# Kernel tuning notes

Hardware: AMD Instinct MI355X
Metric: run time of the kernel (lower is better)

## Reference

```python
import jax, jax.numpy as jnp
import numpy as np


def setup_inputs() -> dict:
    key = jax.random.key(0)
    k1, k2, k3 = jax.random.split(key, 3)
    B, T, F, U = 32, 4096, 512, 512
    x = jax.random.normal(k1, (B, T, F), dtype=jnp.float32)
    W = jax.random.normal(k2, (F, U), dtype=jnp.float32)
    b = jnp.zeros((U,), dtype=jnp.float32)
    V = jax.random.uniform(k3, (U, 1), dtype=jnp.float32)
    return {"x": x, "W": W, "b": b, "V": V}


def reference(x, W, b, V):
    # u = tanh(x @ W + b): [B, T, U]
    u = jnp.tanh(jnp.einsum('btf,fu->btu', x, W) + b)
    # scores = u @ V: [B, T, 1]; softmax over time (dim=1)
    a = jax.nn.softmax(jnp.einsum('btu,uo->bto', u, V), axis=1)
    # weighted sum pooling over time -> [B, F]
    return jnp.sum(x * a, axis=1)
```

## Files before the change

kernel.cpp:

```cpp
#include <hip/hip_runtime.h>


#define XT 4096
#define XF 512
#define XU 512
#define ROWS (32 * 4096)

typedef __attribute__((ext_vector_type(8))) short short8;
typedef __attribute__((ext_vector_type(16))) float f32x16;

__device__ inline void cvt_hilo(float x, unsigned short &h, unsigned short &l) {
  unsigned u = __builtin_bit_cast(unsigned, x);
  h = (unsigned short)(u >> 16);
  float hf = __builtin_bit_cast(float, u & 0xFFFF0000u);
  float lo = x - hf;
  l = (unsigned short)(__builtin_bit_cast(unsigned, lo) >> 16);
}

__device__ inline float tanh_fast(float z) {
  float e = __expf(2.0f * z);
  return 1.0f - 2.0f * __builtin_amdgcn_rcpf(e + 1.0f);
}

__global__ void wconv_kernel(const float *__restrict__ W,
                             unsigned short *__restrict__ whi,
                             unsigned short *__restrict__ wlo) {
  int t2 = blockIdx.x * 256 + threadIdx.x;
  int l = t2 & 31;
  int g = (t2 >> 5) & 1;
  int t = (t2 >> 6) & 15;
  int s = t2 >> 10;
  short8 hv, lv;
#pragma unroll
  for (int j = 0; j < 8; ++j) {
    unsigned short h, lo;
    cvt_hilo(W[(size_t)(s * 16 + g * 8 + j) * XU + t * 32 + l], h, lo);
    hv[j] = (short)h;
    lv[j] = (short)lo;
  }
  size_t off = (size_t)s * 8192 + t * 512 + g * 256 + l * 8;
  *(short8 *)(whi + off) = hv;
  *(short8 *)(wlo + off) = lv;
}

__global__ __launch_bounds__(512, 2)
void gemm_scores_kernel(const float *__restrict__ x,
                        const unsigned short *__restrict__ whi,
                        const unsigned short *__restrict__ wlo,
                        const float *__restrict__ bias,
                        const float *__restrict__ V,
                        float *__restrict__ scores) {
  __shared__ float scb[512];

  const int tid = threadIdx.x;
  const int lane = tid & 63;
  const int wave = tid >> 6;
  const int wr = wave >> 2;
  const int wc = wave & 3;
  const int l31 = lane & 31;
  const int half = lane >> 5;
  const size_t rowbase = (size_t)blockIdx.x * 128;

  f32x16 acc[2][4];
#pragma unroll
  for (int a = 0; a < 2; ++a)
#pragma unroll
    for (int c = 0; c < 4; ++c)
#pragma unroll
      for (int r = 0; r < 16; ++r) acc[a][c][r] = 0.f;

  const float *xr0 = x + (rowbase + wr * 64 + l31) * XF + half * 8;
  const float *xr1 = xr0 + 32 * XF;
  const unsigned short *whp = whi + (size_t)(wc * 4) * 512 + lane * 8;
  const unsigned short *wlp = wlo + (size_t)(wc * 4) * 512 + lane * 8;

#pragma unroll 1
  for (int s = 0; s < 32; ++s) {
    short8 bh[4], bl[4];
    const unsigned short *p = whp + (size_t)s * 8192;
    const unsigned short *q = wlp + (size_t)s * 8192;
#pragma unroll
    for (int cf = 0; cf < 4; ++cf) {
      bh[cf] = *(const short8 *)(p + cf * 512);
      bl[cf] = *(const short8 *)(q + cf * 512);
    }
    float4 a00 = *(const float4 *)(xr0 + s * 16);
    float4 a01 = *(const float4 *)(xr0 + s * 16 + 4);
    float4 a10 = *(const float4 *)(xr1 + s * 16);
    float4 a11 = *(const float4 *)(xr1 + s * 16 + 4);

    short8 ah0, al0, ah1, al1;
    {
      float v0[8] = {a00.x, a00.y, a00.z, a00.w, a01.x, a01.y, a01.z, a01.w};
      float v1[8] = {a10.x, a10.y, a10.z, a10.w, a11.x, a11.y, a11.z, a11.w};
#pragma unroll
      for (int j = 0; j < 8; ++j) {
        unsigned short h, lo;
        cvt_hilo(v0[j], h, lo);
        ah0[j] = (short)h; al0[j] = (short)lo;
        cvt_hilo(v1[j], h, lo);
        ah1[j] = (short)h; al1[j] = (short)lo;
      }
    }

#pragma unroll
    for (int cf = 0; cf < 4; ++cf) {
      acc[0][cf] = __builtin_amdgcn_mfma_f32_32x32x16_bf16(ah0, bh[cf], acc[0][cf], 0, 0, 0);
      acc[1][cf] = __builtin_amdgcn_mfma_f32_32x32x16_bf16(ah1, bh[cf], acc[1][cf], 0, 0, 0);
      acc[0][cf] = __builtin_amdgcn_mfma_f32_32x32x16_bf16(al0, bh[cf], acc[0][cf], 0, 0, 0);
      acc[1][cf] = __builtin_amdgcn_mfma_f32_32x32x16_bf16(al1, bh[cf], acc[1][cf], 0, 0, 0);
      acc[0][cf] = __builtin_amdgcn_mfma_f32_32x32x16_bf16(ah0, bl[cf], acc[0][cf], 0, 0, 0);
      acc[1][cf] = __builtin_amdgcn_mfma_f32_32x32x16_bf16(ah1, bl[cf], acc[1][cf], 0, 0, 0);
    }
  }

  float sc[2][16];
#pragma unroll
  for (int rf = 0; rf < 2; ++rf)
#pragma unroll
    for (int r = 0; r < 16; ++r) sc[rf][r] = 0.f;

#pragma unroll
  for (int cf = 0; cf < 4; ++cf) {
    int n = wc * 128 + cf * 32 + l31;
    float vv = V[n];
    float bb = bias[n];
#pragma unroll
    for (int rf = 0; rf < 2; ++rf)
#pragma unroll
      for (int r = 0; r < 16; ++r)
        sc[rf][r] += tanh_fast(acc[rf][cf][r] + bb) * vv;
  }
#pragma unroll
  for (int m = 1; m <= 16; m <<= 1) {
#pragma unroll
    for (int rf = 0; rf < 2; ++rf)
#pragma unroll
      for (int r = 0; r < 16; ++r)
        sc[rf][r] += __shfl_xor(sc[rf][r], m, 64);
  }
  if (l31 == 0) {
#pragma unroll
    for (int rf = 0; rf < 2; ++rf)
#pragma unroll
      for (int r = 0; r < 16; ++r) {
        int row = wr * 64 + rf * 32 + (r & 3) + 8 * (r >> 2) + 4 * half;
        scb[wc * 128 + row] = sc[rf][r];
      }
  }
  __syncthreads();
  if (tid < 128)
    scores[rowbase + tid] =
        scb[tid] + scb[128 + tid] + scb[256 + tid] + scb[384 + tid];
}

__global__ void stats_kernel(const float *__restrict__ scores,
                             float *__restrict__ stats) {
  int b = blockIdx.x, tid = threadIdx.x;
  const float *s = scores + (size_t)b * XT;
  float v[16];
#pragma unroll
  for (int i = 0; i < 16; ++i) v[i] = s[tid + i * 256];
  float mx = v[0];
#pragma unroll
  for (int i = 1; i < 16; ++i) mx = fmaxf(mx, v[i]);
  for (int m = 1; m < 64; m <<= 1) mx = fmaxf(mx, __shfl_xor(mx, m, 64));
  __shared__ float redm[4], reds[4];
  if ((tid & 63) == 0) redm[tid >> 6] = mx;
  __syncthreads();
  mx = fmaxf(fmaxf(redm[0], redm[1]), fmaxf(redm[2], redm[3]));
  float sum = 0.f;
#pragma unroll
  for (int i = 0; i < 16; ++i) sum += __expf(v[i] - mx);
  for (int m = 1; m < 64; m <<= 1) sum += __shfl_xor(sum, m, 64);
  if ((tid & 63) == 0) reds[tid >> 6] = sum;
  __syncthreads();
  if (tid == 0) {
    stats[b * 2] = mx;
    stats[b * 2 + 1] = reds[0] + reds[1] + reds[2] + reds[3];
  }
}

__global__ __launch_bounds__(256)
void pool_kernel(const float *__restrict__ x, const float *__restrict__ scores,
                 const float *__restrict__ stats, float *__restrict__ out) {
  int b = blockIdx.x >> 5;
  int ch = blockIdx.x & 31;
  int tid = threadIdx.x;
  __shared__ float w[128];
  __shared__ float red[512];
  float mx = stats[b * 2];
  float inv = 1.0f / stats[b * 2 + 1];
  if (tid < 128)
    w[tid] = __expf(scores[(size_t)b * XT + ch * 128 + tid] - mx) * inv;
  __syncthreads();
  int c = tid & 127;
  int ro = tid >> 7;
  const float *xp = x + ((size_t)b * XT + ch * 128) * XF;
  float4 a = {0.f, 0.f, 0.f, 0.f};
#pragma unroll 4
  for (int i = 0; i < 64; ++i) {
    int r = i * 2 + ro;
    float4 v = *(const float4 *)(xp + (size_t)r * XF + c * 4);
    float wv = w[r];
    a.x += wv * v.x;
    a.y += wv * v.y;
    a.z += wv * v.z;
    a.w += wv * v.w;
  }
  if (ro == 1) {
    red[c * 4 + 0] = a.x;
    red[c * 4 + 1] = a.y;
    red[c * 4 + 2] = a.z;
    red[c * 4 + 3] = a.w;
  }
  __syncthreads();
  if (ro == 0) {
    atomicAdd(&out[b * XF + c * 4 + 0], a.x + red[c * 4 + 0]);
    atomicAdd(&out[b * XF + c * 4 + 1], a.y + red[c * 4 + 1]);
    atomicAdd(&out[b * XF + c * 4 + 2], a.z + red[c * 4 + 2]);
    atomicAdd(&out[b * XF + c * 4 + 3], a.w + red[c * 4 + 3]);
  }
}

extern "C" void kernel_launch(void *const *d_in, const int *in_sizes, int n_in,
                              void *d_out, int out_size, void *d_ws,
                              size_t ws_size, hipStream_t stream) {
  const float *x = (const float *)d_in[0];
  const float *W = (const float *)d_in[1];
  const float *bias = (const float *)d_in[2];
  const float *V = (const float *)d_in[3];
  float *out = (float *)d_out;

  unsigned short *whi = (unsigned short *)d_ws;
  unsigned short *wlo = whi + 262144;
  float *scores = (float *)((char *)d_ws + 1048576);
  float *stats = (float *)((char *)d_ws + 1572864);

  hipMemsetAsync(d_out, 0, (size_t)out_size * sizeof(float), stream);
  wconv_kernel<<<128, 256, 0, stream>>>(W, whi, wlo);
  gemm_scores_kernel<<<1024, 512, 0, stream>>>(x, whi, wlo, bias, V, scores);
  stats_kernel<<<32, 256, 0, stream>>>(scores, stats);
  pool_kernel<<<1024, 256, 0, stream>>>(x, scores, stats, out);
}
```

Baseline: 572.9 us.

## Software-pipeline GEMM loads and conversion; halve pool chunk size

The GEMM main loop now double-buffers the W-hi fragments and raw x rows, prefetching step s+1 while issuing MFMAs for step s, and converts x for the next step after the MFMAs. A perm-based cvt_row packs the bf16 hi/lo halves two at a time, and the MFMAs are regrouped by operand. The pool kernel uses 64-row chunks over 2048 blocks for more parallelism, at the cost of twice as many atomics. The extra buffers raise register pressure under the 2-blocks-per-CU launch bound.

```diff
diff --git a/kernel.cpp b/kernel.cpp
--- a/kernel.cpp
+++ b/kernel.cpp
@@ -4,17 +4,40 @@
 #define XT 4096
 #define XF 512
 #define XU 512
-#define ROWS (32 * 4096)
 
 typedef __attribute__((ext_vector_type(8))) short short8;
 typedef __attribute__((ext_vector_type(16))) float f32x16;
+typedef __attribute__((ext_vector_type(4))) unsigned int u32x4;
+
+__device__ inline unsigned fbits(float x) { return __builtin_bit_cast(unsigned, x); }
+__device__ inline float bitsf(unsigned u) { return __builtin_bit_cast(float, u); }
 
 __device__ inline void cvt_hilo(float x, unsigned short &h, unsigned short &l) {
-  unsigned u = __builtin_bit_cast(unsigned, x);
+  unsigned u = fbits(x);
   h = (unsigned short)(u >> 16);
-  float hf = __builtin_bit_cast(float, u & 0xFFFF0000u);
-  float lo = x - hf;
-  l = (unsigned short)(__builtin_bit_cast(unsigned, lo) >> 16);
+  float lo = x - bitsf(u & 0xFFFF0000u);
+  l = (unsigned short)(fbits(lo) >> 16);
+}
+
+__device__ inline unsigned hipack(unsigned a, unsigned b) {
+  return __builtin_amdgcn_perm(b, a, 0x07060302u);
+}
+
+__device__ inline void cvt_row(float4 c0, float4 c1, short8 &h8, short8 &l8) {
+  float f[8] = {c0.x, c0.y, c0.z, c0.w, c1.x, c1.y, c1.z, c1.w};
+  unsigned hp[4], lp[4];
+#pragma unroll
+  for (int p = 0; p < 4; ++p) {
+    unsigned u0 = fbits(f[2 * p]), u1 = fbits(f[2 * p + 1]);
+    hp[p] = hipack(u0, u1);
+    float l0 = f[2 * p] - bitsf(u0 & 0xFFFF0000u);
+    float l1 = f[2 * p + 1] - bitsf(u1 & 0xFFFF0000u);
+    lp[p] = hipack(fbits(l0), fbits(l1));
+  }
+  u32x4 hv = {hp[0], hp[1], hp[2], hp[3]};
+  u32x4 lv = {lp[0], lp[1], lp[2], lp[3]};
+  h8 = __builtin_bit_cast(short8, hv);
+  l8 = __builtin_bit_cast(short8, lv);
 }
 
 __device__ inline float tanh_fast(float z) {
@@ -43,6 +66,8 @@
   *(short8 *)(wlo + off) = lv;
 }
 
+#define MFMA(a, b, c) __builtin_amdgcn_mfma_f32_32x32x16_bf16(a, b, c, 0, 0, 0)
+
 __global__ __launch_bounds__(512, 2)
 void gemm_scores_kernel(const float *__restrict__ x,
                         const unsigned short *__restrict__ whi,
@@ -74,44 +99,51 @@
   const unsigned short *whp = whi + (size_t)(wc * 4) * 512 + lane * 8;
   const unsigned short *wlp = wlo + (size_t)(wc * 4) * 512 + lane * 8;
 
-#pragma unroll 1
+  short8 bh[2][4], bl[4];
+  float4 raw[2][4];
+  short8 ah0, al0, ah1, al1;
+
+#pragma unroll
+  for (int cf = 0; cf < 4; ++cf) bh[0][cf] = *(const short8 *)(whp + cf * 512);
+  raw[0][0] = *(const float4 *)(xr0);
+  raw[0][1] = *(const float4 *)(xr0 + 4);
+  raw[0][2] = *(const float4 *)(xr1);
+  raw[0][3] = *(const float4 *)(xr1 + 4);
+  cvt_row(raw[0][0], raw[0][1], ah0, al0);
+  cvt_row(raw[0][2], raw[0][3], ah1, al1);
+
+#pragma unroll 2
   for (int s = 0; s < 32; ++s) {
-    short8 bh[4], bl[4];
-    const unsigned short *p = whp + (size_t)s * 8192;
-    const unsigned short *q = wlp + (size_t)s * 8192;
+    const int cur = s & 1, nxt = cur ^ 1;
+    const int sn = (s + 1) & 31;
+#pragma unroll
+    for (int cf = 0; cf < 4; ++cf)
+      bl[cf] = *(const short8 *)(wlp + (size_t)s * 8192 + cf * 512);
+#pragma unroll
+    for (int cf = 0; cf < 4; ++cf)
+      bh[nxt][cf] = *(const short8 *)(whp + (size_t)sn * 8192 + cf * 512);
+    raw[nxt][0] = *(const float4 *)(xr0 + sn * 16);
+    raw[nxt][1] = *(const float4 *)(xr0 + sn * 16 + 4);
+    raw[nxt][2] = *(const float4 *)(xr1 + sn * 16);
+    raw[nxt][3] = *(const float4 *)(xr1 + sn * 16 + 4);
+
 #pragma unroll
     for (int cf = 0; cf < 4; ++cf) {
-      bh[cf] = *(const short8 *)(p + cf * 512);
-      bl[cf] = *(const short8 *)(q + cf * 512);
+      acc[0][cf] = MFMA(ah0, bh[cur][cf], acc[0][cf]);
+      acc[1][cf] = MFMA(ah1, bh[cur][cf], acc[1][cf]);
     }
-    float4 a00 = *(const float4 *)(xr0 + s * 16);
-    float4 a01 = *(const float4 *)(xr0 + s * 16 + 4);
-    float4 a10 = *(const float4 *)(xr1 + s * 16);
-    float4 a11 = *(const float4 *)(xr1 + s * 16 + 4);
-
-    short8 ah0, al0, ah1, al1;
-    {
-      float v0[8] = {a00.x, a00.y, a00.z, a00.w, a01.x, a01.y, a01.z, a01.w};
-      float v1[8] = {a10.x, a10.y, a10.z, a10.w, a11.x, a11.y, a11.z, a11.w};
-#pragma unroll
-      for (int j = 0; j < 8; ++j) {
-        unsigned short h, lo;
-        cvt_hilo(v0[j], h, lo);
-        ah0[j] = (short)h; al0[j] = (short)lo;
-        cvt_hilo(v1[j], h, lo);
-        ah1[j] = (short)h; al1[j] = (short)lo;
-      }
+#pragma unroll
+    for (int cf = 0; cf < 4; ++cf) {
+      acc[0][cf] = MFMA(al0, bh[cur][cf], acc[0][cf]);
+      acc[1][cf] = MFMA(al1, bh[cur][cf], acc[1][cf]);
     }
-
 #pragma unroll
     for (int cf = 0; cf < 4; ++cf) {
-      acc[0][cf] = __builtin_amdgcn_mfma_f32_32x32x16_bf16(ah0, bh[cf], acc[0][cf], 0, 0, 0);
-      acc[1][cf] = __builtin_amdgcn_mfma_f32_32x32x16_bf16(ah1, bh[cf], acc[1][cf], 0, 0, 0);
-      acc[0][cf] = __builtin_amdgcn_mfma_f32_32x32x16_bf16(al0, bh[cf], acc[0][cf], 0, 0, 0);
-      acc[1][cf] = __builtin_amdgcn_mfma_f32_32x32x16_bf16(al1, bh[cf], acc[1][cf], 0, 0, 0);
-      acc[0][cf] = __builtin_amdgcn_mfma_f32_32x32x16_bf16(ah0, bl[cf], acc[0][cf], 0, 0, 0);
-      acc[1][cf] = __builtin_amdgcn_mfma_f32_32x32x16_bf16(ah1, bl[cf], acc[1][cf], 0, 0, 0);
+      acc[0][cf] = MFMA(ah0, bl[cf], acc[0][cf]);
+      acc[1][cf] = MFMA(ah1, bl[cf], acc[1][cf]);
     }
+    cvt_row(raw[nxt][0], raw[nxt][1], ah0, al0);
+    cvt_row(raw[nxt][2], raw[nxt][3], ah1, al1);
   }
 
   float sc[2][16];
@@ -184,22 +216,22 @@
 __global__ __launch_bounds__(256)
 void pool_kernel(const float *__restrict__ x, const float *__restrict__ scores,
                  const float *__restrict__ stats, float *__restrict__ out) {
-  int b = blockIdx.x >> 5;
-  int ch = blockIdx.x & 31;
+  int b = blockIdx.x >> 6;
+  int ch = blockIdx.x & 63;
   int tid = threadIdx.x;
-  __shared__ float w[128];
+  __shared__ float w[64];
   __shared__ float red[512];
   float mx = stats[b * 2];
   float inv = 1.0f / stats[b * 2 + 1];
-  if (tid < 128)
-    w[tid] = __expf(scores[(size_t)b * XT + ch * 128 + tid] - mx) * inv;
+  if (tid < 64)
+    w[tid] = __expf(scores[(size_t)b * XT + ch * 64 + tid] - mx) * inv;
   __syncthreads();
   int c = tid & 127;
   int ro = tid >> 7;
-  const float *xp = x + ((size_t)b * XT + ch * 128) * XF;
+  const float *xp = x + ((size_t)b * XT + ch * 64) * XF;
   float4 a = {0.f, 0.f, 0.f, 0.f};
-#pragma unroll 4
-  for (int i = 0; i < 64; ++i) {
+#pragma unroll 8
+  for (int i = 0; i < 32; ++i) {
     int r = i * 2 + ro;
     float4 v = *(const float4 *)(xp + (size_t)r * XF + c * 4);
     float wv = w[r];
@@ -241,5 +273,5 @@
   wconv_kernel<<<128, 256, 0, stream>>>(W, whi, wlo);
   gemm_scores_kernel<<<1024, 512, 0, stream>>>(x, whi, wlo, bias, V, scores);
   stats_kernel<<<32, 256, 0, stream>>>(scores, stats);
-  pool_kernel<<<1024, 256, 0, stream>>>(x, scores, stats, out);
-}
+  pool_kernel<<<2048, 256, 0, stream>>>(x, scores, stats, out);
+}
```

Result: slower. 590.2 us (+3.0%).

## Fuse softmax pooling into GEMM kernel with online-softmax partials and combine

Applied to the files above, without the earlier changes.

The score GEMM kernel now computes a block-local max and exp weights for its 128 rows, then does the weighted pooling over the same x rows while they are likely still in cache. It writes per-block partial sums and (max, sum) stats. A small combine kernel rescales and merges the partials per batch. This removes the separate stats and pool kernels, the second full pass over x from DRAM, the atomics and the memset. In exchange it adds LDS use and a serial reduction inside the GEMM kernel.

```diff
diff --git a/kernel.cpp b/kernel.cpp
--- a/kernel.cpp
+++ b/kernel.cpp
@@ -4,7 +4,6 @@
 #define XT 4096
 #define XF 512
 #define XU 512
-#define ROWS (32 * 4096)
 
 typedef __attribute__((ext_vector_type(8))) short short8;
 typedef __attribute__((ext_vector_type(16))) float f32x16;
@@ -43,14 +42,19 @@
   *(short8 *)(wlo + off) = lv;
 }
 
+#define MFMA(a, b, c) __builtin_amdgcn_mfma_f32_32x32x16_bf16(a, b, c, 0, 0, 0)
+
 __global__ __launch_bounds__(512, 2)
 void gemm_scores_kernel(const float *__restrict__ x,
                         const unsigned short *__restrict__ whi,
                         const unsigned short *__restrict__ wlo,
                         const float *__restrict__ bias,
                         const float *__restrict__ V,
-                        float *__restrict__ scores) {
+                        float *__restrict__ partial,
+                        float *__restrict__ pstats) {
   __shared__ float scb[512];
+  __shared__ float warr[128];
+  __shared__ float red[1536];
 
   const int tid = threadIdx.x;
   const int lane = tid & 63;
@@ -105,12 +109,12 @@
 
 #pragma unroll
     for (int cf = 0; cf < 4; ++cf) {
-      acc[0][cf] = __builtin_amdgcn_mfma_f32_32x32x16_bf16(ah0, bh[cf], acc[0][cf], 0, 0, 0);
-      acc[1][cf] = __builtin_amdgcn_mfma_f32_32x32x16_bf16(ah1, bh[cf], acc[1][cf], 0, 0, 0);
-      acc[0][cf] = __builtin_amdgcn_mfma_f32_32x32x16_bf16(al0, bh[cf], acc[0][cf], 0, 0, 0);
-      acc[1][cf] = __builtin_amdgcn_mfma_f32_32x32x16_bf16(al1, bh[cf], acc[1][cf], 0, 0, 0);
-      acc[0][cf] = __builtin_amdgcn_mfma_f32_32x32x16_bf16(ah0, bl[cf], acc[0][cf], 0, 0, 0);
-      acc[1][cf] = __builtin_amdgcn_mfma_f32_32x32x16_bf16(ah1, bl[cf], acc[1][cf], 0, 0, 0);
+      acc[0][cf] = MFMA(ah0, bh[cf], acc[0][cf]);
+      acc[1][cf] = MFMA(ah1, bh[cf], acc[1][cf]);
+      acc[0][cf] = MFMA(al0, bh[cf], acc[0][cf]);
+      acc[1][cf] = MFMA(al1, bh[cf], acc[1][cf]);
+      acc[0][cf] = MFMA(ah0, bl[cf], acc[0][cf]);
+      acc[1][cf] = MFMA(ah1, bl[cf], acc[1][cf]);
     }
   }
 
@@ -149,78 +153,77 @@
       }
   }
   __syncthreads();
+
+  __shared__ float sarr[128];
   if (tid < 128)
-    scores[rowbase + tid] =
-        scb[tid] + scb[128 + tid] + scb[256 + tid] + scb[384 + tid];
-}
-
-__global__ void stats_kernel(const float *__restrict__ scores,
-                             float *__restrict__ stats) {
-  int b = blockIdx.x, tid = threadIdx.x;
-  const float *s = scores + (size_t)b * XT;
-  float v[16];
-#pragma unroll
-  for (int i = 0; i < 16; ++i) v[i] = s[tid + i * 256];
-  float mx = v[0];
-#pragma unroll
-  for (int i = 1; i < 16; ++i) mx = fmaxf(mx, v[i]);
-  for (int m = 1; m < 64; m <<= 1) mx = fmaxf(mx, __shfl_xor(mx, m, 64));
-  __shared__ float redm[4], reds[4];
-  if ((tid & 63) == 0) redm[tid >> 6] = mx;
-  __syncthreads();
-  mx = fmaxf(fmaxf(redm[0], redm[1]), fmaxf(redm[2], redm[3]));
-  float sum = 0.f;
-#pragma unroll
-  for (int i = 0; i < 16; ++i) sum += __expf(v[i] - mx);
-  for (int m = 1; m < 64; m <<= 1) sum += __shfl_xor(sum, m, 64);
-  if ((tid & 63) == 0) reds[tid >> 6] = sum;
-  __syncthreads();
+    sarr[tid] = scb[tid] + scb[128 + tid] + scb[256 + tid] + scb[384 + tid];
+  __syncthreads();
+  float mloc = -1e30f;
+#pragma unroll 8
+  for (int i = 0; i < 128; ++i) mloc = fmaxf(mloc, sarr[i]);
+  if (tid < 128) warr[tid] = __expf(sarr[tid] - mloc);
+  __syncthreads();
+
+  const int rg = tid >> 7;
+  const int c4 = tid & 127;
+  const float *xp = x + rowbase * XF;
+  float4 pa = {0.f, 0.f, 0.f, 0.f};
+#pragma unroll 8
+  for (int i = 0; i < 32; ++i) {
+    int r = rg * 32 + i;
+    float4 v = *(const float4 *)(xp + (size_t)r * XF + c4 * 4);
+    float wv = warr[r];
+    pa.x += wv * v.x;
+    pa.y += wv * v.y;
+    pa.z += wv * v.z;
+    pa.w += wv * v.w;
+  }
+  if (rg > 0) {
+    float *rp = red + (rg - 1) * 512 + c4 * 4;
+    rp[0] = pa.x; rp[1] = pa.y; rp[2] = pa.z; rp[3] = pa.w;
+  }
+  __syncthreads();
+  if (rg == 0) {
+    const float *r0 = red + c4 * 4;
+    float4 o;
+    o.x = pa.x + r0[0] + r0[512] + r0[1024];
+    o.y = pa.y + r0[1] + r0[513] + r0[1025];
+    o.z = pa.z + r0[2] + r0[514] + r0[1026];
+    o.w = pa.w + r0[3] + r0[515] + r0[1027];
+    *(float4 *)(partial + (size_t)blockIdx.x * 512 + c4 * 4) = o;
+  }
   if (tid == 0) {
-    stats[b * 2] = mx;
-    stats[b * 2 + 1] = reds[0] + reds[1] + reds[2] + reds[3];
-  }
-}
-
-__global__ __launch_bounds__(256)
-void pool_kernel(const float *__restrict__ x, const float *__restrict__ scores,
-                 const float *__restrict__ stats, float *__restrict__ out) {
-  int b = blockIdx.x >> 5;
-  int ch = blockIdx.x & 31;
-  int tid = threadIdx.x;
-  __shared__ float w[128];
-  __shared__ float red[512];
-  float mx = stats[b * 2];
-  float inv = 1.0f / stats[b * 2 + 1];
-  if (tid < 128)
-    w[tid] = __expf(scores[(size_t)b * XT + ch * 128 + tid] - mx) * inv;
-  __syncthreads();
-  int c = tid & 127;
-  int ro = tid >> 7;
-  const float *xp = x + ((size_t)b * XT + ch * 128) * XF;
-  float4 a = {0.f, 0.f, 0.f, 0.f};
-#pragma unroll 4
-  for (int i = 0; i < 64; ++i) {
-    int r = i * 2 + ro;
-    float4 v = *(const float4 *)(xp + (size_t)r * XF + c * 4);
-    float wv = w[r];
-    a.x += wv * v.x;
-    a.y += wv * v.y;
-    a.z += wv * v.z;
-    a.w += wv * v.w;
-  }
-  if (ro == 1) {
-    red[c * 4 + 0] = a.x;
-    red[c * 4 + 1] = a.y;
-    red[c * 4 + 2] = a.z;
-    red[c * 4 + 3] = a.w;
-  }
-  __syncthreads();
-  if (ro == 0) {
-    atomicAdd(&out[b * XF + c * 4 + 0], a.x + red[c * 4 + 0]);
-    atomicAdd(&out[b * XF + c * 4 + 1], a.y + red[c * 4 + 1]);
-    atomicAdd(&out[b * XF + c * 4 + 2], a.z + red[c * 4 + 2]);
-    atomicAdd(&out[b * XF + c * 4 + 3], a.w + red[c * 4 + 3]);
-  }
+    float l = 0.f;
+#pragma unroll 8
+    for (int i = 0; i < 128; ++i) l += warr[i];
+    pstats[blockIdx.x * 2] = mloc;
+    pstats[blockIdx.x * 2 + 1] = l;
+  }
+}
+
+__global__ __launch_bounds__(512)
+void combine_kernel(const float *__restrict__ partial,
+                    const float *__restrict__ pstats,
+                    float *__restrict__ out) {
+  int b = blockIdx.x;
+  int f = threadIdx.x;
+  __shared__ float ml[32], ll[32];
+  if (f < 32) {
+    ml[f] = pstats[(b * 32 + f) * 2];
+    ll[f] = pstats[(b * 32 + f) * 2 + 1];
+  }
+  __syncthreads();
+  float M = -1e30f;
+#pragma unroll
+  for (int c = 0; c < 32; ++c) M = fmaxf(M, ml[c]);
+  float L = 0.f;
+#pragma unroll
+  for (int c = 0; c < 32; ++c) L += __expf(ml[c] - M) * ll[c];
+  float acc = 0.f;
+#pragma unroll
+  for (int c = 0; c < 32; ++c)
+    acc += __expf(ml[c] - M) * partial[(size_t)(b * 32 + c) * 512 + f];
+  out[b * XF + f] = acc / L;
 }
 
 extern "C" void kernel_launch(void *const *d_in, const int *in_sizes, int n_in,
@@ -234,12 +237,11 @@
 
   unsigned short *whi = (unsigned short *)d_ws;
   unsigned short *wlo = whi + 262144;
-  float *scores = (float *)((char *)d_ws + 1048576);
-  float *stats = (float *)((char *)d_ws + 1572864);
-
-  hipMemsetAsync(d_out, 0, (size_t)out_size * sizeof(float), stream);
+  float *partial = (float *)((char *)d_ws + 1048576);
+  float *pstats = (float *)((char *)d_ws + 1048576 + 2097152);
+
   wconv_kernel<<<128, 256, 0, stream>>>(W, whi, wlo);
-  gemm_scores_kernel<<<1024, 512, 0, stream>>>(x, whi, wlo, bias, V, scores);
-  stats_kernel<<<32, 256, 0, stream>>>(scores, stats);
-  pool_kernel<<<1024, 256, 0, stream>>>(x, scores, stats, out);
-}
+  gemm_scores_kernel<<<1024, 512, 0, stream>>>(x, whi, wlo, bias, V, partial,
+                                               pstats);
+  combine_kernel<<<32, 512, 0, stream>>>(partial, pstats, out);
+}
```

New measurement: 568.5 us. About the same (-0.8%).
